# Performance work log

Hardware: AMD Instinct MI355X
Metric: run time of the kernel (lower is better)

The kernel has to match this reference:

```python
import jax, jax.numpy as jnp
import numpy as np

H = 1024        # hidden_size
NH = 16         # num_heads
HD = H // NH    # head_dim
NS = 3          # num_strata


def setup_inputs() -> dict:
    key = jax.random.key(0)
    ks = jax.random.split(key, 12)
    s = 1.0 / np.sqrt(H)
    inp = {
        "hidden_states": jax.random.normal(ks[0], (2, 2048, H), dtype=jnp.float32),
        "Wq": jax.random.uniform(ks[1], (H, H), minval=-s, maxval=s, dtype=jnp.float32),
        "bq": jax.random.uniform(ks[2], (H,), minval=-s, maxval=s, dtype=jnp.float32),
        "Wk": jax.random.uniform(ks[3], (H, H), minval=-s, maxval=s, dtype=jnp.float32),
        "bk": jax.random.uniform(ks[4], (H,), minval=-s, maxval=s, dtype=jnp.float32),
        "Wv": jax.random.uniform(ks[5], (H, H), minval=-s, maxval=s, dtype=jnp.float32),
        "bv": jax.random.uniform(ks[6], (H,), minval=-s, maxval=s, dtype=jnp.float32),
        "Ws": jax.random.uniform(ks[7], (NS, H, H), minval=-s, maxval=s, dtype=jnp.float32),
        "bs": jax.random.uniform(ks[8], (NS, H), minval=-s, maxval=s, dtype=jnp.float32),
        "Wo": jax.random.uniform(ks[9], (H, H), minval=-s, maxval=s, dtype=jnp.float32),
        "bo": jax.random.uniform(ks[10], (H,), minval=-s, maxval=s, dtype=jnp.float32),
    }
    return inp


def reference(hidden_states, Wq, bq, Wk, bk, Wv, bv, Ws, bs, Wo, bo):
    B, S, _ = hidden_states.shape
    # torch nn.Linear: y = x @ W.T + b
    q = hidden_states @ Wq.T + bq
    k = hidden_states @ Wk.T + bk
    v = hidden_states @ Wv.T + bv
    # [B, NH, S, HD]
    q = q.reshape(B, S, NH, HD).transpose(0, 2, 1, 3)
    k = k.reshape(B, S, NH, HD).transpose(0, 2, 1, 3)
    v = v.reshape(B, S, NH, HD).transpose(0, 2, 1, 3)
    scores = jnp.einsum('bhqd,bhkd->bhqk', q, k) / jnp.sqrt(jnp.float32(HD))
    attn = jax.nn.softmax(scores, axis=-1)
    out = jnp.einsum('bhqk,bhkd->bhqd', attn, v)
    attn_output = out.transpose(0, 2, 1, 3).reshape(B, S, H)
    # stratum projections, averaged: [NS, B, S, H] -> mean over strata
    strata = jnp.einsum('bsh,ngh->nbsg', attn_output, Ws) + bs[:, None, None, :]
    enhanced = strata.mean(axis=0)
    output = enhanced @ Wo.T + bo
    return output
```

## Files before the change

### kernel.cpp

```cpp
#include <hip/hip_runtime.h>
#include <stdint.h>

typedef __attribute__((ext_vector_type(8))) short short8;
typedef __attribute__((ext_vector_type(4))) short short4v;
typedef __attribute__((ext_vector_type(4))) float f32x4;
typedef __attribute__((ext_vector_type(16))) float f32x16;
typedef __attribute__((ext_vector_type(2))) unsigned int u32x2;
typedef unsigned int u32;
typedef const __attribute__((address_space(1))) u32* gas_ptr;
typedef __attribute__((address_space(3))) u32* las_ptr;

#define QSCALE 0.18033688011112042f

__device__ inline short f2bf(float x) {
    u32 u = __float_as_uint(x);
    u = u + 0x7FFFu + ((u >> 16) & 1u);
    return (short)(u >> 16);
}
__device__ inline void gload16(const void* g, const void* l) {
    __builtin_amdgcn_global_load_lds((gas_ptr)g, (las_ptr)l, 16, 0, 0);
}

__global__ __launch_bounds__(256) void prep(const float* __restrict__ X,
                                            const float* __restrict__ Wq,
                                            const float* __restrict__ Wk,
                                            const float* __restrict__ Wv,
                                            const float* __restrict__ Wo,
                                            const float* __restrict__ Ws,
                                            const float* __restrict__ bs,
                                            const float* __restrict__ bo,
                                            short* __restrict__ Xb,
                                            short* __restrict__ Wcat,
                                            short* __restrict__ Wob,
                                            short* __restrict__ WmT,
                                            float* __restrict__ bc) {
    __shared__ short T[64][65];
    const int tid = threadIdx.x;
    const int bid = blockIdx.x;
    if (bid < 8192) {
        const float* src;
        short* dst;
        int rel;
        if (bid < 4096)      { src = X;  dst = Xb;                rel = bid; }
        else if (bid < 5120) { src = Wq; dst = Wcat;              rel = bid - 4096; }
        else if (bid < 6144) { src = Wk; dst = Wcat + (1 << 20);  rel = bid - 5120; }
        else if (bid < 7168) { src = Wv; dst = Wcat + (2 << 20);  rel = bid - 6144; }
        else                 { src = Wo; dst = Wob;               rel = bid - 7168; }
        int i = (rel * 256 + tid) * 4;
        float4 v = *(const float4*)&src[i];
        short4v o;
        o[0] = f2bf(v.x); o[1] = f2bf(v.y); o[2] = f2bf(v.z); o[3] = f2bf(v.w);
        *(short4v*)&dst[i] = o;
    } else if (bid < 8448) {
        const int id = bid - 8192;
        const int gx = (id & 15) * 64, jy = (id >> 4) * 64;
        const int HH = 1 << 20;
        for (int e = tid; e < 4096; e += 256) {
            int j = e >> 6, g = e & 63;
            int idx = (jy + j) * 1024 + gx + g;
            float v = (Ws[idx] + Ws[idx + HH] + Ws[idx + 2 * HH]) * (1.0f / 3.0f);
            T[g][j] = f2bf(v);
        }
        __syncthreads();
        for (int e = tid; e < 4096; e += 256) {
            int g = e >> 6, j = e & 63;
            WmT[(long)(gx + g) * 1024 + jy + j] = T[g][j];
        }
    } else {
        const int lane = tid & 63;
        const int n = (bid - 8448) * 4 + (tid >> 6);
        float acc = 0.0f;
        for (int j0 = 0; j0 < 1024; j0 += 64) {
            int j = j0 + lane;
            float bm = (bs[j] + bs[j + 1024] + bs[j + 2048]) * (1.0f / 3.0f);
            acc += Wo[(long)n * 1024 + j] * bm;
        }
#pragma unroll
        for (int off = 1; off < 64; off <<= 1) acc += __shfl_xor(acc, off, 64);
        if (lane == 0) bc[n] = acc + bo[n];
    }
}

__global__ __launch_bounds__(256) void gemm_qkvwc(const short* __restrict__ Xb,
                                                  const short* __restrict__ Wcat,
                                                  const short* __restrict__ Wob,
                                                  const short* __restrict__ WmT,
                                                  const float* __restrict__ bq,
                                                  const float* __restrict__ bk,
                                                  const float* __restrict__ bv,
                                                  short* __restrict__ Qb,
                                                  short* __restrict__ Kb,
                                                  short* __restrict__ Vt,
                                                  short* __restrict__ Wc) {
    __shared__ short As[64 * 64];
    __shared__ short Bs[128 * 64];
    const int K = 1024;
    const int tid  = threadIdx.x;
    const int lane = tid & 63;
    const int wave = tid >> 6;
    const int quad = lane >> 4;
    const int l16  = lane & 15;
    const int bid = blockIdx.x;
    const short *A, *W;
    int m0, n0, sel;
    if (bid < 1536) {
        sel = bid >> 9;
        int r = bid & 511;
        m0 = (r >> 3) * 64;
        n0 = (r & 7) * 128;
        A = Xb;
        W = Wcat + (long)sel * (1 << 20);
    } else {
        int w = bid - 1536;
        sel = 3;
        m0 = (w >> 3) * 64;
        n0 = (w & 7) * 128;
        A = Wob;
        W = WmT;
    }
    const int wm = (wave >> 1) * 32;
    const int wn = (wave & 1) * 64;

    f32x4 acc[2][4] = {};
    const int sr = tid >> 3;
    const int scol = (((tid & 7) ^ (sr & 7)) << 3);
    const int fo_a = ((quad ^ (l16 & 7)) << 3);
    const int fo_b = (((4 + quad) ^ (l16 & 7)) << 3);

    for (int k0 = 0; k0 < K; k0 += 64) {
#pragma unroll
        for (int i = 0; i < 2; i++) {
            int r = i * 32 + sr;
            gload16(&A[(long)(m0 + r) * K + k0 + scol], &As[i * 2048 + wave * 512]);
        }
#pragma unroll
        for (int i = 0; i < 4; i++) {
            int r = i * 32 + sr;
            gload16(&W[(long)(n0 + r) * K + k0 + scol], &Bs[i * 2048 + wave * 512]);
        }
        __syncthreads();
        short8 bfr[4][2];
#pragma unroll
        for (int ni = 0; ni < 4; ni++) {
            const int row = wn + ni * 16 + l16;
            bfr[ni][0] = *(short8*)&Bs[row * 64 + fo_a];
            bfr[ni][1] = *(short8*)&Bs[row * 64 + fo_b];
        }
#pragma unroll
        for (int mi = 0; mi < 2; mi++) {
            const int row = wm + mi * 16 + l16;
            short8 af0 = *(short8*)&As[row * 64 + fo_a];
            short8 af1 = *(short8*)&As[row * 64 + fo_b];
#pragma unroll
            for (int ni = 0; ni < 4; ni++) {
                acc[mi][ni] = __builtin_amdgcn_mfma_f32_16x16x32_bf16(af0, bfr[ni][0],
                                                                      acc[mi][ni], 0, 0, 0);
                acc[mi][ni] = __builtin_amdgcn_mfma_f32_16x16x32_bf16(af1, bfr[ni][1],
                                                                      acc[mi][ni], 0, 0, 0);
            }
        }
        __syncthreads();
    }

#pragma unroll
    for (int mi = 0; mi < 2; mi++) {
#pragma unroll
        for (int ni = 0; ni < 4; ni++) {
            const int n = n0 + wn + ni * 16 + l16;
            const int mbase = m0 + wm + mi * 16 + quad * 4;
            float bv2 = 0.0f;
            if (sel == 0) bv2 = bq[n];
            else if (sel == 1) bv2 = bk[n];
            else if (sel == 2) bv2 = bv[n];
            if (sel == 2) {
                short4v pk;
#pragma unroll
                for (int r = 0; r < 4; r++) pk[r] = f2bf(acc[mi][ni][r] + bv2);
                long addr = ((long)(mbase >> 11) << 21) + (long)n * 2048 + (mbase & 2047);
                *(short4v*)&Vt[addr] = pk;
            } else if (sel == 0) {
#pragma unroll
                for (int r = 0; r < 4; r++)
                    Qb[(long)(mbase + r) * 1024 + n] = f2bf((acc[mi][ni][r] + bv2) * QSCALE);
            } else {
                short* C = (sel == 1) ? Kb : Wc;
#pragma unroll
                for (int r = 0; r < 4; r++)
                    C[(long)(mbase + r) * 1024 + n] = f2bf(acc[mi][ni][r] + bv2);
            }
        }
    }
}

__global__ __launch_bounds__(256) void attn_kernel(const short* __restrict__ Q,
                                                   const short* __restrict__ Kb,
                                                   const short* __restrict__ Vt,
                                                   short* __restrict__ O) {
    __shared__ short Ks[2][64 * 64];
    __shared__ short Vs[64 * 64];
    __shared__ short Ps[4][32 * 64];
    const int tid  = threadIdx.x;
    const int lane = tid & 63;
    const int wave = tid >> 6;
    const int l32  = lane & 31;
    const int hi   = lane >> 5;
    const int sw   = l32 & 7;
    const int q0 = blockIdx.x * 128;
    const int h  = blockIdx.y;
    const int b  = blockIdx.z;

    short8 qB[4];
    {
        const long qbase = (long)(b * 2048 + q0 + wave * 32 + l32) * 1024 + h * 64 + hi * 8;
#pragma unroll
        for (int t = 0; t < 4; t++) qB[t] = *(const short8*)&Q[qbase + t * 16];
    }

    const int sr = tid >> 3;
    const int scol = (((tid & 7) ^ (sr & 7)) << 3);
    const short* Kp = Kb + (long)(b * 2048) * 1024 + h * 64;
    const short* Vp = Vt + ((long)b << 21) + (long)h * 64 * 2048;

    f32x16 o[2] = {};
    float lsum = 0.0f;
    short* const psw = &Ps[wave][0];

#pragma unroll
    for (int i = 0; i < 2; i++) {
        int r = i * 32 + sr;
        gload16(&Kp[(long)r * 1024 + scol], &Ks[0][i * 2048 + wave * 512]);
    }
    __syncthreads();

    for (int kt = 0; kt < 32; kt++) {
        const int cur = kt & 1;
        const int kb = kt * 64;

#pragma unroll
        for (int i = 0; i < 2; i++) {
            int r = i * 32 + sr;
            gload16(&Vp[(long)r * 2048 + kb + scol], &Vs[i * 2048 + wave * 512]);
        }

#pragma unroll
        for (int kvt = 0; kvt < 2; kvt++) {
            const int row = kvt * 32 + l32;
            f32x16 st = {};
#pragma unroll
            for (int step = 0; step < 4; step++) {
                short8 ak = *(short8*)&Ks[cur][row * 64 + (((step * 2 + hi) ^ sw) << 3)];
                st = __builtin_amdgcn_mfma_f32_32x32x16_bf16(ak, qB[step], st, 0, 0, 0);
            }
#pragma unroll
            for (int g = 0; g < 4; g++) {
                float p0 = __builtin_amdgcn_exp2f(st[g * 4 + 0]);
                float p1 = __builtin_amdgcn_exp2f(st[g * 4 + 1]);
                float p2 = __builtin_amdgcn_exp2f(st[g * 4 + 2]);
                float p3 = __builtin_amdgcn_exp2f(st[g * 4 + 3]);
                lsum += (p0 + p1) + (p2 + p3);
                u32 a0 = __float_as_uint(p0) + 0x8000u;
                u32 a1 = __float_as_uint(p1) + 0x8000u;
                u32 a2 = __float_as_uint(p2) + 0x8000u;
                u32 a3 = __float_as_uint(p3) + 0x8000u;
                u32x2 w;
                w[0] = __builtin_amdgcn_perm(a1, a0, 0x07060302u);
                w[1] = __builtin_amdgcn_perm(a3, a2, 0x07060302u);
                *(u32x2*)((char*)psw + l32 * 128 + (((kvt * 4 + g) ^ sw) << 4) + hi * 8) = w;
            }
        }

        short8 pB[4];
#pragma unroll
        for (int step = 0; step < 4; step++)
            pB[step] = *(short8*)&psw[l32 * 64 + (((step * 2 + hi) ^ sw) << 3)];

        __syncthreads();

        if (kt < 31) {
            const int kbn = kb + 64;
#pragma unroll
            for (int i = 0; i < 2; i++) {
                int r = i * 32 + sr;
                gload16(&Kp[(long)(kbn + r) * 1024 + scol],
                        &Ks[cur ^ 1][i * 2048 + wave * 512]);
            }
        }

#pragma unroll
        for (int dt = 0; dt < 2; dt++) {
            const int row = dt * 32 + l32;
#pragma unroll
            for (int step = 0; step < 4; step++) {
                short8 av = *(short8*)&Vs[row * 64 + (((step * 2 + hi) ^ sw) << 3)];
                o[dt] = __builtin_amdgcn_mfma_f32_32x32x16_bf16(av, pB[step], o[dt], 0, 0, 0);
            }
        }

        __syncthreads();
    }

    lsum += __shfl_xor(lsum, 32, 64);
    const float inv = 1.0f / lsum;
    const long rbase = (long)(b * 2048 + q0 + wave * 32 + l32) * 1024 + h * 64;
#pragma unroll
    for (int dt = 0; dt < 2; dt++) {
#pragma unroll
        for (int g = 0; g < 4; g++) {
            short4v pk;
#pragma unroll
            for (int i = 0; i < 4; i++) pk[i] = f2bf(o[dt][g * 4 + i] * inv);
            *(short4v*)&O[rbase + dt * 32 + g * 8 + hi * 4] = pk;
        }
    }
}

__global__ __launch_bounds__(256) void gemm_final(const short* __restrict__ A,
                                                  const short* __restrict__ W,
                                                  const float* __restrict__ bias,
                                                  float* __restrict__ C) {
    __shared__ short As[64 * 64];
    __shared__ short Bs[128 * 64];
    const int K = 1024;
    const int tid  = threadIdx.x;
    const int lane = tid & 63;
    const int wave = tid >> 6;
    const int quad = lane >> 4;
    const int l16  = lane & 15;
    const int bid = blockIdx.x;
    const int m0 = (bid >> 3) * 64;
    const int n0 = (bid & 7) * 128;
    const int wm = (wave >> 1) * 32;
    const int wn = (wave & 1) * 64;

    f32x4 acc[2][4] = {};
    const int sr = tid >> 3;
    const int scol = (((tid & 7) ^ (sr & 7)) << 3);
    const int fo_a = ((quad ^ (l16 & 7)) << 3);
    const int fo_b = (((4 + quad) ^ (l16 & 7)) << 3);

    for (int k0 = 0; k0 < K; k0 += 64) {
#pragma unroll
        for (int i = 0; i < 2; i++) {
            int r = i * 32 + sr;
            gload16(&A[(long)(m0 + r) * K + k0 + scol], &As[i * 2048 + wave * 512]);
        }
#pragma unroll
        for (int i = 0; i < 4; i++) {
            int r = i * 32 + sr;
            gload16(&W[(long)(n0 + r) * K + k0 + scol], &Bs[i * 2048 + wave * 512]);
        }
        __syncthreads();
        short8 bfr[4][2];
#pragma unroll
        for (int ni = 0; ni < 4; ni++) {
            const int row = wn + ni * 16 + l16;
            bfr[ni][0] = *(short8*)&Bs[row * 64 + fo_a];
            bfr[ni][1] = *(short8*)&Bs[row * 64 + fo_b];
        }
#pragma unroll
        for (int mi = 0; mi < 2; mi++) {
            const int row = wm + mi * 16 + l16;
            short8 af0 = *(short8*)&As[row * 64 + fo_a];
            short8 af1 = *(short8*)&As[row * 64 + fo_b];
#pragma unroll
            for (int ni = 0; ni < 4; ni++) {
                acc[mi][ni] = __builtin_amdgcn_mfma_f32_16x16x32_bf16(af0, bfr[ni][0],
                                                                      acc[mi][ni], 0, 0, 0);
                acc[mi][ni] = __builtin_amdgcn_mfma_f32_16x16x32_bf16(af1, bfr[ni][1],
                                                                      acc[mi][ni], 0, 0, 0);
            }
        }
        __syncthreads();
    }

#pragma unroll
    for (int mi = 0; mi < 2; mi++) {
#pragma unroll
        for (int ni = 0; ni < 4; ni++) {
            const int n = n0 + wn + ni * 16 + l16;
            const float bv = bias[n];
            const int mbase = m0 + wm + mi * 16 + quad * 4;
#pragma unroll
            for (int r = 0; r < 4; r++)
                C[(long)(mbase + r) * 1024 + n] = acc[mi][ni][r] + bv;
        }
    }
}

extern "C" void kernel_launch(void* const* d_in, const int* in_sizes, int n_in,
                              void* d_out, int out_size, void* d_ws, size_t ws_size,
                              hipStream_t stream) {
    const float* X  = (const float*)d_in[0];
    const float* Wq = (const float*)d_in[1];
    const float* bq = (const float*)d_in[2];
    const float* Wk = (const float*)d_in[3];
    const float* bk = (const float*)d_in[4];
    const float* Wv = (const float*)d_in[5];
    const float* bv = (const float*)d_in[6];
    const float* Ws = (const float*)d_in[7];
    const float* bs = (const float*)d_in[8];
    const float* Wo = (const float*)d_in[9];
    const float* bo = (const float*)d_in[10];

    char* ws = (char*)d_ws;
    const long MB = 1 << 20;
    short* Xb   = (short*)(ws + 0 * MB);
    short* Wcat = (short*)(ws + 8 * MB);
    short* WmT  = (short*)(ws + 14 * MB);
    short* Wob  = (short*)(ws + 16 * MB);
    short* Wc   = (short*)(ws + 18 * MB);
    float* bc   = (float*)(ws + 20 * MB);
    short* Qb   = (short*)(ws + 21 * MB);
    short* Kbf  = (short*)(ws + 29 * MB);
    short* Vtb  = (short*)(ws + 37 * MB);
    short* AO   = Xb;

    dim3 bb(256);

    prep<<<dim3(8704), bb, 0, stream>>>(X, Wq, Wk, Wv, Wo, Ws, bs, bo,
                                        Xb, Wcat, Wob, WmT, bc);
    gemm_qkvwc<<<dim3(1664), bb, 0, stream>>>(Xb, Wcat, Wob, WmT, bq, bk, bv,
                                              Qb, Kbf, Vtb, Wc);
    attn_kernel<<<dim3(16, 16, 2), bb, 0, stream>>>(Qb, Kbf, Vtb, AO);
    gemm_final<<<dim3(512), bb, 0, stream>>>(AO, Wc, bc, (float*)d_out);
}
```

Baseline: 216.8 us.

## Split attention over two KV halves and merge partials in a combine kernel

The attention kernel now splits the key/value sequence into two halves, doubling the grid so more blocks are available to fill the GPU's compute units. Each block writes its own softmax-normalized partial output in bf16 along with its row sum. A new combine kernel merges the two halves, weighting each by its share of the total row sum. The cost is an extra launch, extra global traffic for the partial outputs, and an additional bf16 rounding of the intermediate results.

```diff
diff --git a/kernel.cpp b/kernel.cpp
--- a/kernel.cpp
+++ b/kernel.cpp
@@ -16,6 +16,9 @@
     u32 u = __float_as_uint(x);
     u = u + 0x7FFFu + ((u >> 16) & 1u);
     return (short)(u >> 16);
+}
+__device__ inline float bf2f(short b) {
+    return __uint_as_float(((u32)(unsigned short)b) << 16);
 }
 __device__ inline void gload16(const void* g, const void* l) {
     __builtin_amdgcn_global_load_lds((gas_ptr)g, (las_ptr)l, 16, 0, 0);
@@ -195,7 +198,8 @@
 __global__ __launch_bounds__(256) void attn_kernel(const short* __restrict__ Q,
                                                    const short* __restrict__ Kb,
                                                    const short* __restrict__ Vt,
-                                                   short* __restrict__ O) {
+                                                   short* __restrict__ Pp,
+                                                   float* __restrict__ L) {
     __shared__ short Ks[2][64 * 64];
     __shared__ short Vs[64 * 64];
     __shared__ short Ps[4][32 * 64];
@@ -205,9 +209,12 @@
     const int l32  = lane & 31;
     const int hi   = lane >> 5;
     const int sw   = l32 & 7;
-    const int q0 = blockIdx.x * 128;
+    const int qt    = blockIdx.x & 15;
+    const int split = blockIdx.x >> 4;
+    const int q0 = qt * 128;
     const int h  = blockIdx.y;
     const int b  = blockIdx.z;
+    const int kt0 = split * 16;
 
     short8 qB[4];
     {
@@ -228,13 +235,13 @@
 #pragma unroll
     for (int i = 0; i < 2; i++) {
         int r = i * 32 + sr;
-        gload16(&Kp[(long)r * 1024 + scol], &Ks[0][i * 2048 + wave * 512]);
+        gload16(&Kp[(long)(kt0 * 64 + r) * 1024 + scol], &Ks[0][i * 2048 + wave * 512]);
     }
     __syncthreads();
 
-    for (int kt = 0; kt < 32; kt++) {
-        const int cur = kt & 1;
-        const int kb = kt * 64;
+    for (int t = 0; t < 16; t++) {
+        const int cur = t & 1;
+        const int kb = (kt0 + t) * 64;
 
 #pragma unroll
         for (int i = 0; i < 2; i++) {
@@ -276,7 +283,7 @@
 
         __syncthreads();
 
-        if (kt < 31) {
+        if (t < 15) {
             const int kbn = kb + 64;
 #pragma unroll
             for (int i = 0; i < 2; i++) {
@@ -301,7 +308,9 @@
 
     lsum += __shfl_xor(lsum, 32, 64);
     const float inv = 1.0f / lsum;
-    const long rbase = (long)(b * 2048 + q0 + wave * 32 + l32) * 1024 + h * 64;
+    const int q = q0 + wave * 32 + l32;
+    if (hi == 0) L[split * 65536 + (b * 16 + h) * 2048 + q] = lsum;
+    const long rbase = (long)split * 4194304 + (long)(b * 2048 + q) * 1024 + h * 64;
 #pragma unroll
     for (int dt = 0; dt < 2; dt++) {
 #pragma unroll
@@ -309,9 +318,30 @@
             short4v pk;
 #pragma unroll
             for (int i = 0; i < 4; i++) pk[i] = f2bf(o[dt][g * 4 + i] * inv);
-            *(short4v*)&O[rbase + dt * 32 + g * 8 + hi * 4] = pk;
-        }
-    }
+            *(short4v*)&Pp[rbase + dt * 32 + g * 8 + hi * 4] = pk;
+        }
+    }
+}
+
+__global__ __launch_bounds__(256) void combine(const short* __restrict__ Pp,
+                                               const float* __restrict__ L,
+                                               short* __restrict__ AO) {
+    const int row = blockIdx.x;
+    const int b = row >> 11, q = row & 2047;
+    const int col = threadIdx.x * 4;
+    const int h = col >> 6;
+    const float l1 = L[(b * 16 + h) * 2048 + q];
+    const float l2 = L[65536 + (b * 16 + h) * 2048 + q];
+    const float inv = 1.0f / (l1 + l2);
+    const float w1 = l1 * inv, w2 = l2 * inv;
+    const long idx = (long)row * 1024 + col;
+    short4v p1 = *(const short4v*)&Pp[idx];
+    short4v p2 = *(const short4v*)&Pp[4194304 + idx];
+    short4v ov;
+#pragma unroll
+    for (int i = 0; i < 4; i++)
+        ov[i] = f2bf(bf2f(p1[i]) * w1 + bf2f(p2[i]) * w2);
+    *(short4v*)&AO[idx] = ov;
 }
 
 __global__ __launch_bounds__(256) void gemm_final(const short* __restrict__ A,
@@ -413,6 +443,8 @@
     short* Qb   = (short*)(ws + 21 * MB);
     short* Kbf  = (short*)(ws + 29 * MB);
     short* Vtb  = (short*)(ws + 37 * MB);
+    short* Pp   = (short*)(ws + 45 * MB);
+    float* L    = (float*)(ws + 61 * MB);
     short* AO   = Xb;
 
     dim3 bb(256);
@@ -421,6 +453,7 @@
                                         Xb, Wcat, Wob, WmT, bc);
     gemm_qkvwc<<<dim3(1664), bb, 0, stream>>>(Xb, Wcat, Wob, WmT, bq, bk, bv,
                                               Qb, Kbf, Vtb, Wc);
-    attn_kernel<<<dim3(16, 16, 2), bb, 0, stream>>>(Qb, Kbf, Vtb, AO);
+    attn_kernel<<<dim3(32, 16, 2), bb, 0, stream>>>(Qb, Kbf, Vtb, Pp, L);
+    combine<<<dim3(4096), bb, 0, stream>>>(Pp, L, AO);
     gemm_final<<<dim3(512), bb, 0, stream>>>(AO, Wc, bc, (float*)d_out);
 }
```

Result: slower. 222.6 us (+2.7%).
